# Kernel optimization log

Measured on AMD Instinct MI355X. Metric: run time of the kernel, lower is better.

Reference implementation:

```python
import jax, jax.numpy as jnp
import numpy as np

N, E = 100000, 1600000
IN, HID, OUT = 128, 64, 64
BN_EPS = 1e-5


def setup_inputs() -> dict:
    key = jax.random.key(0)
    ks = jax.random.split(key, 6)
    x = jax.random.normal(ks[0], (N, IN), dtype=jnp.float32)
    edge_index = jax.random.randint(ks[1], (2, E), 0, N, dtype=jnp.int32)
    W1 = jax.random.normal(ks[2], (IN, HID), dtype=jnp.float32) / np.sqrt(IN).astype(np.float32)
    b1 = jnp.zeros((HID,), jnp.float32)
    bn_weight = jnp.ones((HID,), jnp.float32)
    bn_bias = jnp.zeros((HID,), jnp.float32)
    W2 = jax.random.normal(ks[3], (HID, OUT), dtype=jnp.float32) / np.sqrt(HID).astype(np.float32)
    b2 = jnp.zeros((OUT,), jnp.float32)
    return {"x": x, "edge_index": edge_index, "W1": W1, "b1": b1,
            "bn_weight": bn_weight, "bn_bias": bn_bias, "W2": W2, "b2": b2}


def _gcn_conv(x, W, b, src, dst, deg_inv_sqrt):
    # PyG GCNConv: linear first, then symmetric-normalized aggregation with self-loops.
    h = x @ W                                        # [N, out]
    norm = deg_inv_sqrt[src] * deg_inv_sqrt[dst]     # [E]
    agg = jax.ops.segment_sum(h[src] * norm[:, None], dst, num_segments=h.shape[0])
    # self-loop contribution: norm = 1/deg
    agg = agg + h * (deg_inv_sqrt * deg_inv_sqrt)[:, None]
    return agg + b


def reference(x, edge_index, W1, b1, bn_weight, bn_bias, W2, b2):
    src, dst = edge_index[0], edge_index[1]
    # degree including self-loop (GCNConv add_self_loops=True, edge_weight=1)
    deg = jax.ops.segment_sum(jnp.ones((E,), x.dtype), dst, num_segments=N) + 1.0
    deg_inv_sqrt = jax.lax.rsqrt(deg)
    h = _gcn_conv(x, W1, b1, src, dst, deg_inv_sqrt)
    # BatchNorm1d (training-mode batch statistics, biased variance)
    mean = jnp.mean(h, axis=0)
    var = jnp.var(h, axis=0)
    h = (h - mean) * jax.lax.rsqrt(var + BN_EPS) * bn_weight + bn_bias
    h = jax.nn.relu(h)
    # dropout: inference mode (identity)
    return _gcn_conv(h, W2, b2, src, dst, deg_inv_sqrt)
```

## Files before the change

kernel.cpp:

```cpp
#include <hip/hip_runtime.h>

#define N_NODES 100000
#define E_EDGES 1600000
#define IN_F    128
#define HID_F   64
#define OUT_F   64
#define BN_EPS  1e-5f
#define NBUK    391
#define CHUNK   6250
#define NGBLK   3125
#define NMBLK   1563

typedef __bf16 bf16x8 __attribute__((ext_vector_type(8)));
typedef float  f32x4  __attribute__((ext_vector_type(4)));

__device__ __forceinline__ float bflo(unsigned int u) { return __uint_as_float(u << 16); }
__device__ __forceinline__ float bfhi(unsigned int u) { return __uint_as_float(u & 0xFFFF0000u); }
__device__ __forceinline__ unsigned int pack2bf(float a, float b) {
    unsigned int ua = __float_as_uint(a), ub = __float_as_uint(b);
    ua = (ua + 0x7fffu + ((ua >> 16) & 1u)) >> 16;
    ub = (ub + 0x7fffu + ((ub >> 16) & 1u)) >> 16;
    return ua | (ub << 16);
}
__device__ __forceinline__ unsigned short bf1(float a) {
    unsigned int ua = __float_as_uint(a);
    return (unsigned short)((ua + 0x7fffu + ((ua >> 16) & 1u)) >> 16);
}
#define ADD8(A, u)                                           \
    do {                                                     \
        A[0] += bflo((u).x); A[1] += bfhi((u).x);            \
        A[2] += bflo((u).y); A[3] += bfhi((u).y);            \
        A[4] += bflo((u).z); A[5] += bfhi((u).z);            \
        A[6] += bflo((u).w); A[7] += bfhi((u).w);            \
    } while (0)

__global__ __launch_bounds__(512) void k_chist(const int* __restrict__ dstv,
                                               int* __restrict__ chist) {
    __shared__ int h[NBUK];
    const int tid = threadIdx.x;
    const int e0 = blockIdx.x * CHUNK;
    for (int b = tid; b < NBUK; b += 512) h[b] = 0;
    __syncthreads();
    for (int t = tid; t < CHUNK; t += 512)
        atomicAdd(&h[dstv[e0 + t] >> 8], 1);
    __syncthreads();
    for (int b = tid; b < NBUK; b += 512)
        if (h[b]) atomicAdd(&chist[b], h[b]);
}

__global__ __launch_bounds__(512) void k_cscan(int* __restrict__ coff,
                                               int* __restrict__ ccur) {
    __shared__ int sh[512];
    const int tid = threadIdx.x;
    int v = (tid < NBUK) ? coff[tid] : 0;
    sh[tid] = v;
    __syncthreads();
    for (int off = 1; off < 512; off <<= 1) {
        int t = (tid >= off) ? sh[tid - off] : 0;
        __syncthreads();
        sh[tid] += t;
        __syncthreads();
    }
    int excl = sh[tid] - v;
    if (tid < NBUK) { coff[tid] = excl; ccur[tid] = excl; }
    if (tid == 0) coff[NBUK] = E_EDGES;
}

__global__ __launch_bounds__(512) void k_bucket(const int* __restrict__ srcv,
                                                const int* __restrict__ dstv,
                                                int* __restrict__ ccur,
                                                unsigned int* __restrict__ aux) {
    __shared__ int dl[CHUNK];
    __shared__ int hist[NBUK], base[NBUK], lcur[NBUK];
    const int tid = threadIdx.x;
    const int e0 = blockIdx.x * CHUNK;
    for (int b = tid; b < NBUK; b += 512) hist[b] = 0;
    __syncthreads();
    for (int t = tid; t < CHUNK; t += 512) {
        int d = dstv[e0 + t];
        dl[t] = d;
        atomicAdd(&hist[d >> 8], 1);
    }
    __syncthreads();
    for (int b = tid; b < NBUK; b += 512) {
        int h = hist[b];
        if (h) base[b] = atomicAdd(&ccur[b], h);
        lcur[b] = 0;
    }
    __syncthreads();
    for (int t = tid; t < CHUNK; t += 512) {
        int d = dl[t];
        int b = d >> 8;
        int off = atomicAdd(&lcur[b], 1);
        aux[base[b] + off] = ((unsigned int)srcv[e0 + t] << 8) | (unsigned int)(d & 255);
    }
}

__global__ __launch_bounds__(256) void k_csrnode(const int* __restrict__ coff,
                                                 const unsigned int* __restrict__ aux,
                                                 int* __restrict__ rowptr,
                                                 float* __restrict__ dis,
                                                 int* __restrict__ csr_src) {
    __shared__ int c0[256], sc[256], cur[256];
    const int tid = threadIdx.x;
    const int n0 = blockIdx.x * 256;
    const int nn = min(256, N_NODES - n0);
    const int estart = coff[blockIdx.x];
    const int eend   = coff[blockIdx.x + 1];
    c0[tid] = 0;
    __syncthreads();
    for (int e = estart + tid; e < eend; e += 256)
        atomicAdd(&c0[aux[e] & 255], 1);
    __syncthreads();
    int v = c0[tid];
    sc[tid] = v;
    __syncthreads();
    for (int off = 1; off < 256; off <<= 1) {
        int t = (tid >= off) ? sc[tid - off] : 0;
        __syncthreads();
        sc[tid] += t;
        __syncthreads();
    }
    int excl = sc[tid] - v;
    if (tid < nn) {
        int p = estart + excl;
        rowptr[n0 + tid] = p;
        cur[tid] = p;
        dis[n0 + tid] = rsqrtf((float)v + 1.0f);
    }
    if (blockIdx.x == NBUK - 1 && tid == 0) rowptr[N_NODES] = E_EDGES;
    __syncthreads();
    for (int e = estart + tid; e < eend; e += 256) {
        unsigned int u = aux[e];
        int pos = atomicAdd(&cur[u & 255], 1);
        csr_src[pos] = (int)(u >> 8);
    }
}

__global__ __launch_bounds__(256) void k_gemm1(const float* __restrict__ x,
                                               const float* __restrict__ W1,
                                               const float* __restrict__ dis,
                                               unsigned short* __restrict__ hs1) {
    __shared__ unsigned short Asb[64 * 136];
    __shared__ unsigned short Btb[64 * 136];
    __shared__ unsigned short Cc[64 * 72];
    __shared__ float disS[64];
    const int tid = threadIdx.x;
    const int r0 = blockIdx.x * 64;

    if (tid < 64) disS[tid] = (r0 + tid < N_NODES) ? dis[r0 + tid] : 0.f;

    const float4* x4 = (const float4*)x;
#pragma unroll
    for (int p = 0; p < 4; ++p) {
        int idx8 = p * 256 + tid;
        int row = idx8 >> 4, c8 = idx8 & 15;
        float4 v0 = make_float4(0.f, 0.f, 0.f, 0.f), v1 = v0;
        if (r0 + row < N_NODES) {
            v0 = x4[(size_t)(r0 + row) * 32 + c8 * 2];
            v1 = x4[(size_t)(r0 + row) * 32 + c8 * 2 + 1];
        }
        uint4 u;
        u.x = pack2bf(v0.x, v0.y); u.y = pack2bf(v0.z, v0.w);
        u.z = pack2bf(v1.x, v1.y); u.w = pack2bf(v1.z, v1.w);
        *(uint4*)&Asb[row * 136 + c8 * 8] = u;
    }
    for (int idx = tid; idx < IN_F * HID_F; idx += 256) {
        int k = idx >> 6, n = idx & 63;
        Btb[n * 136 + k] = bf1(W1[idx]);
    }
    __syncthreads();

    const int wv = tid >> 6, lane = tid & 63;
    const int m = lane & 15, quad = lane >> 4;
    const int arow = wv * 16 + m;
    f32x4 acc[4] = {};
#pragma unroll
    for (int ks = 0; ks < 4; ++ks) {
        int k0 = ks * 32 + quad * 8;
        bf16x8 af = *(const bf16x8*)&Asb[arow * 136 + k0];
#pragma unroll
        for (int c = 0; c < 4; ++c) {
            bf16x8 bfr = *(const bf16x8*)&Btb[(c * 16 + m) * 136 + k0];
            acc[c] = __builtin_amdgcn_mfma_f32_16x16x32_bf16(af, bfr, acc[c], 0, 0, 0);
        }
    }
#pragma unroll
    for (int c = 0; c < 4; ++c)
#pragma unroll
        for (int r = 0; r < 4; ++r) {
            int rl = wv * 16 + quad * 4 + r;
            Cc[rl * 72 + c * 16 + m] = bf1(acc[c][r] * disS[rl]);
        }
    __syncthreads();
#pragma unroll
    for (int p = 0; p < 2; ++p) {
        int idx = p * 256 + tid;
        int row = idx >> 3, c8 = idx & 7;
        if (r0 + row < N_NODES)
            *(uint4*)&hs1[(size_t)(r0 + row) * 64 + c8 * 8] = *(uint4*)&Cc[row * 72 + c8 * 8];
    }
}

__global__ __launch_bounds__(256) void k_gather1(const int* __restrict__ rowptr,
                                                 const int* __restrict__ csr_src,
                                                 const unsigned short* __restrict__ hsb,
                                                 const float* __restrict__ dis,
                                                 const float* __restrict__ b1,
                                                 float* __restrict__ agg,
                                                 float* __restrict__ partials) {
    const int tid = threadIdx.x;
    const int g = tid >> 3, q = tid & 7;
    const int n = blockIdx.x * 32 + g;
    const uint4* __restrict__ hs16 = (const uint4*)hsb;

    const int start = rowptr[n], end = rowptr[n + 1];
    float A0[8] = {}, A1[8] = {}, A2[8] = {}, A3[8] = {};
    {
        uint4 u = hs16[(size_t)n * 8 + q];
        ADD8(A0, u);
    }
    int i = start;
    for (; i + 3 < end; i += 4) {
        int s0 = csr_src[i + 0], s1 = csr_src[i + 1];
        int s2 = csr_src[i + 2], s3 = csr_src[i + 3];
        uint4 u0 = hs16[(size_t)s0 * 8 + q];
        uint4 u1 = hs16[(size_t)s1 * 8 + q];
        uint4 u2 = hs16[(size_t)s2 * 8 + q];
        uint4 u3 = hs16[(size_t)s3 * 8 + q];
        ADD8(A0, u0); ADD8(A1, u1); ADD8(A2, u2); ADD8(A3, u3);
    }
    for (; i < end; ++i) {
        uint4 u = hs16[(size_t)csr_src[i] * 8 + q];
        ADD8(A0, u);
    }
    const float d = dis[n];
    const float4 blo = ((const float4*)b1)[q * 2];
    const float4 bhi = ((const float4*)b1)[q * 2 + 1];
    float o[8];
    o[0] = fmaf(d, A0[0] + A1[0] + A2[0] + A3[0], blo.x);
    o[1] = fmaf(d, A0[1] + A1[1] + A2[1] + A3[1], blo.y);
    o[2] = fmaf(d, A0[2] + A1[2] + A2[2] + A3[2], blo.z);
    o[3] = fmaf(d, A0[3] + A1[3] + A2[3] + A3[3], blo.w);
    o[4] = fmaf(d, A0[4] + A1[4] + A2[4] + A3[4], bhi.x);
    o[5] = fmaf(d, A0[5] + A1[5] + A2[5] + A3[5], bhi.y);
    o[6] = fmaf(d, A0[6] + A1[6] + A2[6] + A3[6], bhi.z);
    o[7] = fmaf(d, A0[7] + A1[7] + A2[7] + A3[7], bhi.w);
    float4* ag = (float4*)(agg + (size_t)n * HID_F + q * 8);
    ag[0] = make_float4(o[0], o[1], o[2], o[3]);
    ag[1] = make_float4(o[4], o[5], o[6], o[7]);

    __shared__ float4 redA[256], redB[256];
    redA[tid] = make_float4(o[0], o[1], o[2], o[3]);
    redB[tid] = make_float4(o[4], o[5], o[6], o[7]);
    __syncthreads();
    for (int s = 128; s >= 8; s >>= 1) {
        if (tid < s) {
            redA[tid].x += redA[tid + s].x; redA[tid].y += redA[tid + s].y;
            redA[tid].z += redA[tid + s].z; redA[tid].w += redA[tid + s].w;
            redB[tid].x += redB[tid + s].x; redB[tid].y += redB[tid + s].y;
            redB[tid].z += redB[tid + s].z; redB[tid].w += redB[tid + s].w;
        }
        __syncthreads();
    }
    float4* pr = (float4*)(partials + (size_t)blockIdx.x * 128);
    if (tid < 8) { pr[tid * 2] = redA[tid]; pr[tid * 2 + 1] = redB[tid]; }
    __syncthreads();
    redA[tid] = make_float4(o[0] * o[0], o[1] * o[1], o[2] * o[2], o[3] * o[3]);
    redB[tid] = make_float4(o[4] * o[4], o[5] * o[5], o[6] * o[6], o[7] * o[7]);
    __syncthreads();
    for (int s = 128; s >= 8; s >>= 1) {
        if (tid < s) {
            redA[tid].x += redA[tid + s].x; redA[tid].y += redA[tid + s].y;
            redA[tid].z += redA[tid + s].z; redA[tid].w += redA[tid + s].w;
            redB[tid].x += redB[tid + s].x; redB[tid].y += redB[tid + s].y;
            redB[tid].z += redB[tid + s].z; redB[tid].w += redB[tid + s].w;
        }
        __syncthreads();
    }
    if (tid < 8) { pr[16 + tid * 2] = redA[tid]; pr[16 + tid * 2 + 1] = redB[tid]; }
}

__global__ __launch_bounds__(256) void k_bnfinal(const float* __restrict__ partials,
                                                 float* __restrict__ bnstats) {
    const int tid = threadIdx.x;
    const int col = tid & 127;
    const int half = tid >> 7;
    float s = 0.f;
    for (int r = blockIdx.x * 2 + half; r < NGBLK; r += 128)
        s += partials[(size_t)r * 128 + col];
    __shared__ float sh[256];
    sh[tid] = s;
    __syncthreads();
    if (tid < 128) unsafeAtomicAdd(&bnstats[col], sh[tid] + sh[tid + 128]);
}

__global__ __launch_bounds__(256) void k_gemm2(const float* __restrict__ agg1,
                                               const float* __restrict__ W2,
                                               const float* __restrict__ dis,
                                               const float* __restrict__ bnw,
                                               const float* __restrict__ bnb,
                                               const float* __restrict__ bnstats,
                                               unsigned short* __restrict__ hs2) {
    __shared__ unsigned short Ab[64 * 72];
    __shared__ unsigned short Bt2[64 * 72];
    __shared__ unsigned short Cc[64 * 72];
    __shared__ float scale_s[64], shift_s[64], disS[64];
    const int tid = threadIdx.x;
    const int r0 = blockIdx.x * 64;

    if (tid < 64) {
        const float invN = 1.0f / (float)N_NODES;
        float mean = bnstats[tid] * invN;
        float var  = bnstats[64 + tid] * invN - mean * mean;
        float sc   = bnw[tid] * rsqrtf(var + BN_EPS);
        scale_s[tid] = sc;
        shift_s[tid] = fmaf(-mean, sc, bnb[tid]);
        disS[tid] = (r0 + tid < N_NODES) ? dis[r0 + tid] : 0.f;
    }
    for (int idx = tid; idx < HID_F * OUT_F; idx += 256) {
        int k = idx >> 6, n = idx & 63;
        Bt2[n * 72 + k] = bf1(W2[idx]);
    }
    __syncthreads();

    const float4* a4 = (const float4*)agg1;
#pragma unroll
    for (int p = 0; p < 4; ++p) {
        int idx4 = p * 256 + tid;
        int row = idx4 >> 4, c4 = idx4 & 15;
        float4 v = make_float4(0.f, 0.f, 0.f, 0.f);
        if (r0 + row < N_NODES) v = a4[(size_t)(r0 + row) * 16 + c4];
        int k0 = c4 * 4;
        v.x = fmaxf(fmaf(v.x, scale_s[k0 + 0], shift_s[k0 + 0]), 0.f);
        v.y = fmaxf(fmaf(v.y, scale_s[k0 + 1], shift_s[k0 + 1]), 0.f);
        v.z = fmaxf(fmaf(v.z, scale_s[k0 + 2], shift_s[k0 + 2]), 0.f);
        v.w = fmaxf(fmaf(v.w, scale_s[k0 + 3], shift_s[k0 + 3]), 0.f);
        uint2 u;
        u.x = pack2bf(v.x, v.y); u.y = pack2bf(v.z, v.w);
        *(uint2*)&Ab[row * 72 + c4 * 4] = u;
    }
    __syncthreads();

    const int wv = tid >> 6, lane = tid & 63;
    const int m = lane & 15, quad = lane >> 4;
    const int arow = wv * 16 + m;
    f32x4 acc[4] = {};
#pragma unroll
    for (int ks = 0; ks < 2; ++ks) {
        int k0 = ks * 32 + quad * 8;
        bf16x8 af = *(const bf16x8*)&Ab[arow * 72 + k0];
#pragma unroll
        for (int c = 0; c < 4; ++c) {
            bf16x8 bfr = *(const bf16x8*)&Bt2[(c * 16 + m) * 72 + k0];
            acc[c] = __builtin_amdgcn_mfma_f32_16x16x32_bf16(af, bfr, acc[c], 0, 0, 0);
        }
    }
#pragma unroll
    for (int c = 0; c < 4; ++c)
#pragma unroll
        for (int r = 0; r < 4; ++r) {
            int rl = wv * 16 + quad * 4 + r;
            Cc[rl * 72 + c * 16 + m] = bf1(acc[c][r] * disS[rl]);
        }
    __syncthreads();
#pragma unroll
    for (int p = 0; p < 2; ++p) {
        int idx = p * 256 + tid;
        int row = idx >> 3, c8 = idx & 7;
        if (r0 + row < N_NODES)
            *(uint4*)&hs2[(size_t)(r0 + row) * 64 + c8 * 8] = *(uint4*)&Cc[row * 72 + c8 * 8];
    }
}

__global__ __launch_bounds__(256) void k_gather2(const int* __restrict__ rowptr,
                                                 const int* __restrict__ csr_src,
                                                 const unsigned short* __restrict__ hsb,
                                                 const float* __restrict__ dis,
                                                 const float* __restrict__ b2,
                                                 float* __restrict__ out) {
    const int tid = threadIdx.x;
    const int g = tid >> 3, q = tid & 7;
    const int n = blockIdx.x * 32 + g;
    const uint4* __restrict__ hs16 = (const uint4*)hsb;

    const int start = rowptr[n], end = rowptr[n + 1];
    float A0[8] = {}, A1[8] = {}, A2[8] = {}, A3[8] = {};
    {
        uint4 u = hs16[(size_t)n * 8 + q];
        ADD8(A0, u);
    }
    int i = start;
    for (; i + 3 < end; i += 4) {
        int s0 = csr_src[i + 0], s1 = csr_src[i + 1];
        int s2 = csr_src[i + 2], s3 = csr_src[i + 3];
        uint4 u0 = hs16[(size_t)s0 * 8 + q];
        uint4 u1 = hs16[(size_t)s1 * 8 + q];
        uint4 u2 = hs16[(size_t)s2 * 8 + q];
        uint4 u3 = hs16[(size_t)s3 * 8 + q];
        ADD8(A0, u0); ADD8(A1, u1); ADD8(A2, u2); ADD8(A3, u3);
    }
    for (; i < end; ++i) {
        uint4 u = hs16[(size_t)csr_src[i] * 8 + q];
        ADD8(A0, u);
    }
    const float d = dis[n];
    const float4 blo = ((const float4*)b2)[q * 2];
    const float4 bhi = ((const float4*)b2)[q * 2 + 1];
    float4 o0, o1;
    o0.x = fmaf(d, A0[0] + A1[0] + A2[0] + A3[0], blo.x);
    o0.y = fmaf(d, A0[1] + A1[1] + A2[1] + A3[1], blo.y);
    o0.z = fmaf(d, A0[2] + A1[2] + A2[2] + A3[2], blo.z);
    o0.w = fmaf(d, A0[3] + A1[3] + A2[3] + A3[3], blo.w);
    o1.x = fmaf(d, A0[4] + A1[4] + A2[4] + A3[4], bhi.x);
    o1.y = fmaf(d, A0[5] + A1[5] + A2[5] + A3[5], bhi.y);
    o1.z = fmaf(d, A0[6] + A1[6] + A2[6] + A3[6], bhi.z);
    o1.w = fmaf(d, A0[7] + A1[7] + A2[7] + A3[7], bhi.w);
    float4* op = (float4*)(out + (size_t)n * OUT_F + q * 8);
    op[0] = o0;
    op[1] = o1;
}

extern "C" void kernel_launch(void* const* d_in, const int* in_sizes, int n_in,
                              void* d_out, int out_size, void* d_ws, size_t ws_size,
                              hipStream_t stream) {
    const float* x   = (const float*)d_in[0];
    const int*   ei  = (const int*)d_in[1];
    const float* W1  = (const float*)d_in[2];
    const float* b1  = (const float*)d_in[3];
    const float* bnw = (const float*)d_in[4];
    const float* bnb = (const float*)d_in[5];
    const float* W2  = (const float*)d_in[6];
    const float* b2  = (const float*)d_in[7];
    float* out = (float*)d_out;

    float* ws = (float*)d_ws;
    float*        dis     = ws;
    int*          rowptr  = (int*)(ws + 100352);
    int*          coff    = (int*)(ws + 100352 + 100608);
    int*          ccur    = (int*)(ws + 100352 + 100608 + 512);
    float*        bnstats = ws + 100352 + 100608 + 512 + 512;
    int*          csr_src = (int*)(ws + 100352 + 100608 + 512 + 512 + 128);
    float*        bufA    = ws + 100352 + 100608 + 512 + 512 + 128 + 1600000;
    float*        bufB    = bufA + (size_t)N_NODES * HID_F;
    unsigned int*  aux  = (unsigned int*)bufA;
    unsigned short* hsb = (unsigned short*)bufA;
    float* partials = out;

    const int* srcv = ei;
    const int* dstv = ei + E_EDGES;

    hipMemsetAsync(coff, 0, (NBUK + 1) * sizeof(int), stream);
    hipMemsetAsync(bnstats, 0, 128 * sizeof(float), stream);

    k_chist  <<<256, 512, 0, stream>>>(dstv, coff);
    k_cscan  <<<1, 512, 0, stream>>>(coff, ccur);
    k_bucket <<<256, 512, 0, stream>>>(srcv, dstv, ccur, aux);
    k_csrnode<<<NBUK, 256, 0, stream>>>(coff, aux, rowptr, dis, csr_src);

    k_gemm1  <<<NMBLK, 256, 0, stream>>>(x, W1, dis, hsb);
    k_gather1<<<NGBLK, 256, 0, stream>>>(rowptr, csr_src, hsb, dis, b1, bufB, partials);
    k_bnfinal<<<64, 256, 0, stream>>>(partials, bnstats);
    k_gemm2  <<<NMBLK, 256, 0, stream>>>(bufB, W2, dis, bnw, bnb, bnstats, hsb);
    k_gather2<<<NGBLK, 256, 0, stream>>>(rowptr, csr_src, hsb, dis, b2, out);
}
```

Measured before the change: 254.6 us.

## Fuse CSR build into one cooperative kernel and store layer-1 output as bf16

```diff
diff --git a/kernel.cpp b/kernel.cpp
--- a/kernel.cpp
+++ b/kernel.cpp
@@ -1,4 +1,6 @@
 #include <hip/hip_runtime.h>
+#include <hip/hip_cooperative_groups.h>
+namespace cg = cooperative_groups;
 
 #define N_NODES 100000
 #define E_EDGES 1600000
@@ -7,7 +9,7 @@
 #define OUT_F   64
 #define BN_EPS  1e-5f
 #define NBUK    391
-#define CHUNK   6250
+#define CHUNK_C 4093
 #define NGBLK   3125
 #define NMBLK   1563
 
@@ -34,105 +36,105 @@
         A[6] += bflo((u).w); A[7] += bfhi((u).w);            \
     } while (0)
 
-__global__ __launch_bounds__(512) void k_chist(const int* __restrict__ dstv,
-                                               int* __restrict__ chist) {
-    __shared__ int h[NBUK];
-    const int tid = threadIdx.x;
-    const int e0 = blockIdx.x * CHUNK;
-    for (int b = tid; b < NBUK; b += 512) h[b] = 0;
-    __syncthreads();
-    for (int t = tid; t < CHUNK; t += 512)
-        atomicAdd(&h[dstv[e0 + t] >> 8], 1);
-    __syncthreads();
-    for (int b = tid; b < NBUK; b += 512)
-        if (h[b]) atomicAdd(&chist[b], h[b]);
-}
-
-__global__ __launch_bounds__(512) void k_cscan(int* __restrict__ coff,
-                                               int* __restrict__ ccur) {
-    __shared__ int sh[512];
-    const int tid = threadIdx.x;
-    int v = (tid < NBUK) ? coff[tid] : 0;
-    sh[tid] = v;
-    __syncthreads();
-    for (int off = 1; off < 512; off <<= 1) {
-        int t = (tid >= off) ? sh[tid - off] : 0;
+__global__ __launch_bounds__(512) void k_csr(const int* __restrict__ srcv,
+                                             const int* __restrict__ dstv,
+                                             int* __restrict__ coff,
+                                             int* __restrict__ ccur,
+                                             unsigned int* __restrict__ aux,
+                                             int* __restrict__ rowptr,
+                                             float* __restrict__ dis,
+                                             int* __restrict__ csr_src,
+                                             float* __restrict__ bnstats) {
+    cg::grid_group grid = cg::this_grid();
+    __shared__ int dl[CHUNK_C];
+    __shared__ int hA[NBUK], hB[NBUK], hC[NBUK];
+    const int tid = threadIdx.x;
+    const int b = blockIdx.x;
+    const int e0 = b * CHUNK_C;
+    const int e1 = min(E_EDGES, e0 + CHUNK_C);
+
+    if (tid == 0) { coff[b] = 0; if (b == 0) coff[NBUK] = 0; }
+    if (b == 1 && tid < 128) bnstats[tid] = 0.f;
+    grid.sync();
+
+    for (int i = tid; i < NBUK; i += 512) hA[i] = 0;
+    __syncthreads();
+    for (int e = e0 + tid; e < e1; e += 512)
+        atomicAdd(&hA[dstv[e] >> 8], 1);
+    __syncthreads();
+    for (int i = tid; i < NBUK; i += 512)
+        if (hA[i]) atomicAdd(&coff[i], hA[i]);
+    grid.sync();
+
+    if (b == 0) {
+        int v = (tid < NBUK) ? coff[tid] : 0;
+        dl[tid] = v;
         __syncthreads();
-        sh[tid] += t;
+        for (int off = 1; off < 512; off <<= 1) {
+            int t = (tid >= off) ? dl[tid - off] : 0;
+            __syncthreads();
+            dl[tid] += t;
+            __syncthreads();
+        }
+        int excl = dl[tid] - v;
+        if (tid < NBUK) { coff[tid] = excl; ccur[tid] = excl; }
+        if (tid == 0) coff[NBUK] = E_EDGES;
+    }
+    grid.sync();
+
+    for (int i = tid; i < NBUK; i += 512) hA[i] = 0;
+    __syncthreads();
+    for (int e = e0 + tid; e < e1; e += 512) {
+        int d = dstv[e];
+        dl[e - e0] = d;
+        atomicAdd(&hA[d >> 8], 1);
+    }
+    __syncthreads();
+    for (int i = tid; i < NBUK; i += 512) {
+        int h = hA[i];
+        hB[i] = h ? atomicAdd(&ccur[i], h) : 0;
+        hC[i] = 0;
+    }
+    __syncthreads();
+    for (int e = e0 + tid; e < e1; e += 512) {
+        int d = dl[e - e0];
+        int bk = d >> 8;
+        int off = atomicAdd(&hC[bk], 1);
+        aux[hB[bk] + off] = ((unsigned int)srcv[e] << 8) | (unsigned int)(d & 255);
+    }
+    grid.sync();
+
+    const int n0 = b << 8;
+    const int nn = min(256, N_NODES - n0);
+    const int estart = coff[b], eend = coff[b + 1];
+    if (tid < 256) hA[tid] = 0;
+    __syncthreads();
+    for (int e = estart + tid; e < eend; e += 512)
+        atomicAdd(&hA[aux[e] & 255], 1);
+    __syncthreads();
+    if (tid < 256) hB[tid] = hA[tid];
+    __syncthreads();
+    for (int off = 1; off < 256; off <<= 1) {
+        int t = 0;
+        if (tid < 256 && tid >= off) t = hB[tid - off];
         __syncthreads();
-    }
-    int excl = sh[tid] - v;
-    if (tid < NBUK) { coff[tid] = excl; ccur[tid] = excl; }
-    if (tid == 0) coff[NBUK] = E_EDGES;
-}
-
-__global__ __launch_bounds__(512) void k_bucket(const int* __restrict__ srcv,
-                                                const int* __restrict__ dstv,
-                                                int* __restrict__ ccur,
-                                                unsigned int* __restrict__ aux) {
-    __shared__ int dl[CHUNK];
-    __shared__ int hist[NBUK], base[NBUK], lcur[NBUK];
-    const int tid = threadIdx.x;
-    const int e0 = blockIdx.x * CHUNK;
-    for (int b = tid; b < NBUK; b += 512) hist[b] = 0;
-    __syncthreads();
-    for (int t = tid; t < CHUNK; t += 512) {
-        int d = dstv[e0 + t];
-        dl[t] = d;
-        atomicAdd(&hist[d >> 8], 1);
-    }
-    __syncthreads();
-    for (int b = tid; b < NBUK; b += 512) {
-        int h = hist[b];
-        if (h) base[b] = atomicAdd(&ccur[b], h);
-        lcur[b] = 0;
-    }
-    __syncthreads();
-    for (int t = tid; t < CHUNK; t += 512) {
-        int d = dl[t];
-        int b = d >> 8;
-        int off = atomicAdd(&lcur[b], 1);
-        aux[base[b] + off] = ((unsigned int)srcv[e0 + t] << 8) | (unsigned int)(d & 255);
-    }
-}
-
-__global__ __launch_bounds__(256) void k_csrnode(const int* __restrict__ coff,
-                                                 const unsigned int* __restrict__ aux,
-                                                 int* __restrict__ rowptr,
-                                                 float* __restrict__ dis,
-                                                 int* __restrict__ csr_src) {
-    __shared__ int c0[256], sc[256], cur[256];
-    const int tid = threadIdx.x;
-    const int n0 = blockIdx.x * 256;
-    const int nn = min(256, N_NODES - n0);
-    const int estart = coff[blockIdx.x];
-    const int eend   = coff[blockIdx.x + 1];
-    c0[tid] = 0;
-    __syncthreads();
-    for (int e = estart + tid; e < eend; e += 256)
-        atomicAdd(&c0[aux[e] & 255], 1);
-    __syncthreads();
-    int v = c0[tid];
-    sc[tid] = v;
-    __syncthreads();
-    for (int off = 1; off < 256; off <<= 1) {
-        int t = (tid >= off) ? sc[tid - off] : 0;
+        if (tid < 256) hB[tid] += t;
         __syncthreads();
-        sc[tid] += t;
-        __syncthreads();
-    }
-    int excl = sc[tid] - v;
-    if (tid < nn) {
-        int p = estart + excl;
-        rowptr[n0 + tid] = p;
-        cur[tid] = p;
-        dis[n0 + tid] = rsqrtf((float)v + 1.0f);
-    }
-    if (blockIdx.x == NBUK - 1 && tid == 0) rowptr[N_NODES] = E_EDGES;
-    __syncthreads();
-    for (int e = estart + tid; e < eend; e += 256) {
+    }
+    if (tid < 256) {
+        int v = hA[tid];
+        int p = estart + hB[tid] - v;
+        hC[tid] = p;
+        if (tid < nn) {
+            rowptr[n0 + tid] = p;
+            dis[n0 + tid] = rsqrtf((float)v + 1.0f);
+        }
+    }
+    if (b == NBUK - 1 && tid == 0) rowptr[N_NODES] = E_EDGES;
+    __syncthreads();
+    for (int e = estart + tid; e < eend; e += 512) {
         unsigned int u = aux[e];
-        int pos = atomicAdd(&cur[u & 255], 1);
+        int pos = atomicAdd(&hC[u & 255], 1);
         csr_src[pos] = (int)(u >> 8);
     }
 }
@@ -207,7 +209,7 @@
                                                  const unsigned short* __restrict__ hsb,
                                                  const float* __restrict__ dis,
                                                  const float* __restrict__ b1,
-                                                 float* __restrict__ agg,
+                                                 unsigned short* __restrict__ aggb,
                                                  float* __restrict__ partials) {
     const int tid = threadIdx.x;
     const int g = tid >> 3, q = tid & 7;
@@ -246,9 +248,10 @@
     o[5] = fmaf(d, A0[5] + A1[5] + A2[5] + A3[5], bhi.y);
     o[6] = fmaf(d, A0[6] + A1[6] + A2[6] + A3[6], bhi.z);
     o[7] = fmaf(d, A0[7] + A1[7] + A2[7] + A3[7], bhi.w);
-    float4* ag = (float4*)(agg + (size_t)n * HID_F + q * 8);
-    ag[0] = make_float4(o[0], o[1], o[2], o[3]);
-    ag[1] = make_float4(o[4], o[5], o[6], o[7]);
+    uint4 ob;
+    ob.x = pack2bf(o[0], o[1]); ob.y = pack2bf(o[2], o[3]);
+    ob.z = pack2bf(o[4], o[5]); ob.w = pack2bf(o[6], o[7]);
+    ((uint4*)aggb)[(size_t)n * 8 + q] = ob;
 
     __shared__ float4 redA[256], redB[256];
     redA[tid] = make_float4(o[0], o[1], o[2], o[3]);
@@ -295,7 +298,7 @@
     if (tid < 128) unsafeAtomicAdd(&bnstats[col], sh[tid] + sh[tid + 128]);
 }
 
-__global__ __launch_bounds__(256) void k_gemm2(const float* __restrict__ agg1,
+__global__ __launch_bounds__(256) void k_gemm2(const unsigned short* __restrict__ aggb,
                                                const float* __restrict__ W2,
                                                const float* __restrict__ dis,
                                                const float* __restrict__ bnw,
@@ -324,21 +327,29 @@
     }
     __syncthreads();
 
-    const float4* a4 = (const float4*)agg1;
-#pragma unroll
-    for (int p = 0; p < 4; ++p) {
-        int idx4 = p * 256 + tid;
-        int row = idx4 >> 4, c4 = idx4 & 15;
-        float4 v = make_float4(0.f, 0.f, 0.f, 0.f);
-        if (r0 + row < N_NODES) v = a4[(size_t)(r0 + row) * 16 + c4];
-        int k0 = c4 * 4;
-        v.x = fmaxf(fmaf(v.x, scale_s[k0 + 0], shift_s[k0 + 0]), 0.f);
-        v.y = fmaxf(fmaf(v.y, scale_s[k0 + 1], shift_s[k0 + 1]), 0.f);
-        v.z = fmaxf(fmaf(v.z, scale_s[k0 + 2], shift_s[k0 + 2]), 0.f);
-        v.w = fmaxf(fmaf(v.w, scale_s[k0 + 3], shift_s[k0 + 3]), 0.f);
-        uint2 u;
-        u.x = pack2bf(v.x, v.y); u.y = pack2bf(v.z, v.w);
-        *(uint2*)&Ab[row * 72 + c4 * 4] = u;
+    const uint4* a16 = (const uint4*)aggb;
+#pragma unroll
+    for (int p = 0; p < 2; ++p) {
+        int idx = p * 256 + tid;
+        int row = idx >> 3, q = idx & 7;
+        uint4 u = make_uint4(0, 0, 0, 0);
+        if (r0 + row < N_NODES) u = a16[(size_t)(r0 + row) * 8 + q];
+        int k0 = q * 8;
+        float v[8];
+        v[0] = bflo(u.x); v[1] = bfhi(u.x); v[2] = bflo(u.y); v[3] = bfhi(u.y);
+        v[4] = bflo(u.z); v[5] = bfhi(u.z); v[6] = bflo(u.w); v[7] = bfhi(u.w);
+        uint4 o;
+        float w0 = fmaxf(fmaf(v[0], scale_s[k0 + 0], shift_s[k0 + 0]), 0.f);
+        float w1 = fmaxf(fmaf(v[1], scale_s[k0 + 1], shift_s[k0 + 1]), 0.f);
+        float w2 = fmaxf(fmaf(v[2], scale_s[k0 + 2], shift_s[k0 + 2]), 0.f);
+        float w3 = fmaxf(fmaf(v[3], scale_s[k0 + 3], shift_s[k0 + 3]), 0.f);
+        float w4 = fmaxf(fmaf(v[4], scale_s[k0 + 4], shift_s[k0 + 4]), 0.f);
+        float w5 = fmaxf(fmaf(v[5], scale_s[k0 + 5], shift_s[k0 + 5]), 0.f);
+        float w6 = fmaxf(fmaf(v[6], scale_s[k0 + 6], shift_s[k0 + 6]), 0.f);
+        float w7 = fmaxf(fmaf(v[7], scale_s[k0 + 7], shift_s[k0 + 7]), 0.f);
+        o.x = pack2bf(w0, w1); o.y = pack2bf(w2, w3);
+        o.z = pack2bf(w4, w5); o.w = pack2bf(w6, w7);
+        *(uint4*)&Ab[row * 72 + q * 8] = o;
     }
     __syncthreads();
 
@@ -443,24 +454,24 @@
     int*          csr_src = (int*)(ws + 100352 + 100608 + 512 + 512 + 128);
     float*        bufA    = ws + 100352 + 100608 + 512 + 512 + 128 + 1600000;
     float*        bufB    = bufA + (size_t)N_NODES * HID_F;
-    unsigned int*  aux  = (unsigned int*)bufA;
-    unsigned short* hsb = (unsigned short*)bufA;
+    unsigned int*   aux  = (unsigned int*)bufA;
+    unsigned short* hsb  = (unsigned short*)bufA;
+    unsigned short* aggb = (unsigned short*)bufB;
     float* partials = out;
 
     const int* srcv = ei;
     const int* dstv = ei + E_EDGES;
 
-    hipMemsetAsync(coff, 0, (NBUK + 1) * sizeof(int), stream);
-    hipMemsetAsync(bnstats, 0, 128 * sizeof(float), stream);
-
-    k_chist  <<<256, 512, 0, stream>>>(dstv, coff);
-    k_cscan  <<<1, 512, 0, stream>>>(coff, ccur);
-    k_bucket <<<256, 512, 0, stream>>>(srcv, dstv, ccur, aux);
-    k_csrnode<<<NBUK, 256, 0, stream>>>(coff, aux, rowptr, dis, csr_src);
+    {
+        void* args[] = {(void*)&srcv, (void*)&dstv, (void*)&coff, (void*)&ccur,
+                        (void*)&aux, (void*)&rowptr, (void*)&dis, (void*)&csr_src,
+                        (void*)&bnstats};
+        hipLaunchCooperativeKernel((void*)k_csr, dim3(NBUK), dim3(512), args, 0, stream);
+    }
 
     k_gemm1  <<<NMBLK, 256, 0, stream>>>(x, W1, dis, hsb);
-    k_gather1<<<NGBLK, 256, 0, stream>>>(rowptr, csr_src, hsb, dis, b1, bufB, partials);
+    k_gather1<<<NGBLK, 256, 0, stream>>>(rowptr, csr_src, hsb, dis, b1, aggb, partials);
     k_bnfinal<<<64, 256, 0, stream>>>(partials, bnstats);
-    k_gemm2  <<<NMBLK, 256, 0, stream>>>(bufB, W2, dis, bnw, bnb, bnstats, hsb);
+    k_gemm2  <<<NMBLK, 256, 0, stream>>>(aggb, W2, dis, bnw, bnb, bnstats, hsb);
     k_gather2<<<NGBLK, 256, 0, stream>>>(rowptr, csr_src, hsb, dis, b2, out);
 }
```

New measurement: 441.5 us. +73.4%, slower.
